# Optimization experiments

Measured on AMD Instinct MI355X. Metric: run time of the kernel, lower is better.

## Reference

```python
import jax, jax.numpy as jnp
import numpy as np

HEADS = 1
EPS = 1e-12  # torch F.normalize eps


def dwt_haar(x):
    # Haar analysis, J=1, zero mode (even H,W -> no padding needed).
    b, c, H, W = x.shape
    xr = x.reshape(b, c, H // 2, 2, W // 2, 2)
    a = xr[:, :, :, 0, :, 0]
    bb = xr[:, :, :, 0, :, 1]
    cc = xr[:, :, :, 1, :, 0]
    d = xr[:, :, :, 1, :, 1]
    ll = (a + bb + cc + d) * 0.5
    h1 = (a - bb + cc - d) * 0.5  # high in width
    h2 = (a + bb - cc - d) * 0.5  # high in height
    h3 = (a - bb - cc + d) * 0.5  # diagonal
    return ll, h1, h2, h3


def idwt_haar(ll, h1, h2, h3):
    a = (ll + h1 + h2 + h3) * 0.5
    bb = (ll - h1 + h2 - h3) * 0.5
    cc = (ll + h1 - h2 - h3) * 0.5
    d = (ll - h1 - h2 + h3) * 0.5
    row0 = jnp.stack([a, bb], axis=-1)   # (b,c,h2,w2,2)
    row1 = jnp.stack([cc, d], axis=-1)
    y = jnp.stack([row0, row1], axis=3)  # (b,c,h2,2,w2,2)
    b_, c_, h2_, _, w2_, _ = y.shape
    return y.reshape(b_, c_, h2_ * 2, w2_ * 2)


def conv1x1(x, w, bias):
    # x: (b,c,h,w); w: (o,c); bias: (o,)
    return jnp.einsum('oc,bchw->bohw', w, x) + bias[None, :, None, None]


def mdta(x, qw, qb, kw, kb, vw, vb, pw, pb, temp):
    b, c, h, w = x.shape
    q = conv1x1(x, qw, qb).reshape(b, HEADS, c // HEADS, h * w)
    k = conv1x1(x, kw, kb).reshape(b, HEADS, c // HEADS, h * w)
    v = conv1x1(x, vw, vb).reshape(b, HEADS, c // HEADS, h * w)
    q = q / jnp.maximum(jnp.linalg.norm(q, axis=-1, keepdims=True), EPS)
    k = k / jnp.maximum(jnp.linalg.norm(k, axis=-1, keepdims=True), EPS)
    attn = jnp.einsum('bhcn,bhdn->bhcd', q, k) * temp[None]
    attn = jax.nn.softmax(attn, axis=-1)
    out = jnp.einsum('bhcd,bhdn->bhcn', attn, v).reshape(b, c, h, w)
    return conv1x1(out, pw, pb)


def setup_inputs() -> dict:
    key = jax.random.key(0)
    ks = jax.random.split(key, 20)
    B, C, H, W = 16, 64, 256, 256
    C3 = 3 * C
    s1 = 1.0 / np.sqrt(C)
    s3 = 1.0 / np.sqrt(C3)
    d = {'img': jax.random.normal(ks[0], (B, C, H, W), jnp.float32)}
    names = ['qw', 'qb', 'kw', 'kb', 'vw', 'vb', 'pw', 'pb']
    for i, n in enumerate(names):
        if n.endswith('w'):
            d['ll_' + n] = jax.random.normal(ks[1 + i], (C, C), jnp.float32) * s1
            d['h_' + n] = jax.random.normal(ks[10 + i], (C3, C3), jnp.float32) * s3
        else:
            d['ll_' + n] = jax.random.normal(ks[1 + i], (C,), jnp.float32) * s1
            d['h_' + n] = jax.random.normal(ks[10 + i], (C3,), jnp.float32) * s3
    d['ll_temp'] = jnp.ones((HEADS, 1, 1), jnp.float32)
    d['h_temp'] = jnp.ones((HEADS, 1, 1), jnp.float32)
    return d


def reference(img, ll_qw, ll_qb, ll_kw, ll_kb, ll_vw, ll_vb, ll_pw, ll_pb, ll_temp,
              h_qw, h_qb, h_kw, h_kb, h_vw, h_vb, h_pw, h_pb, h_temp):
    b, c, H, W = img.shape
    ll, h1, h2, h3 = dwt_haar(img)
    # rearrange 'b c fp h w -> b (c fp) h w' with fp=3 (bands interleaved per channel)
    hh = jnp.stack([h1, h2, h3], axis=2).reshape(b, c * 3, H // 2, W // 2)
    ll = mdta(ll, ll_qw, ll_qb, ll_kw, ll_kb, ll_vw, ll_vb, ll_pw, ll_pb, ll_temp)
    hh = mdta(hh, h_qw, h_qb, h_kw, h_kb, h_vw, h_vb, h_pw, h_pb, h_temp)
    hh = hh.reshape(b, c, 3, H // 2, W // 2)
    return idwt_haar(ll, hh[:, :, 0], hh[:, :, 1], hh[:, :, 2])
```

## Files before the change

kernel.cpp:

```cpp
#include <hip/hip_runtime.h>

typedef __bf16 bf16;
typedef bf16 bf16x8 __attribute__((ext_vector_type(8)));
typedef bf16 bf16x4 __attribute__((ext_vector_type(4)));
typedef float f32x4 __attribute__((ext_vector_type(4)));

#define NB 16
#define CLL 64
#define CHH 192
#define NPIX 16384
#define SL (CLL * CLL)
#define SH (CHH * CHH)

__global__ __launch_bounds__(256) void k_dwt(const float* __restrict__ img, bf16* __restrict__ xll,
                      bf16* __restrict__ xhh, float* __restrict__ sll, float* __restrict__ shh) {
    int bc = blockIdx.y;
    int b = bc >> 6, c = bc & 63;
    int t = threadIdx.x;
    int r = blockIdx.x * 16 + (t >> 4);
    int q = t & 15;
    const float* p0 = img + ((size_t)bc << 16) + (size_t)(2 * r) * 256 + 16 * q;
    const float* p1 = p0 + 256;
    float4 e0[4], e1[4];
    #pragma unroll
    for (int l = 0; l < 4; l++) { e0[l] = ((const float4*)p0)[l]; e1[l] = ((const float4*)p1)[l]; }
    const float* f0 = (const float*)e0;
    const float* f1 = (const float*)e1;
    bf16x8 vll, v1, v2, v3;
    float s0 = 0.f, s1 = 0.f, s2 = 0.f, s3 = 0.f;
    #pragma unroll
    for (int p = 0; p < 8; p++) {
        float a = f0[2 * p], bb = f0[2 * p + 1], cc = f1[2 * p], d = f1[2 * p + 1];
        float wll = (a + bb + cc + d) * 0.5f;
        float w1  = (a - bb + cc - d) * 0.5f;
        float w2  = (a + bb - cc - d) * 0.5f;
        float w3  = (a - bb - cc + d) * 0.5f;
        vll[p] = (bf16)wll; v1[p] = (bf16)w1; v2[p] = (bf16)w2; v3[p] = (bf16)w3;
        s0 += wll; s1 += w1; s2 += w2; s3 += w3;
    }
    size_t n = (size_t)r * 128 + 8 * q;
    *(bf16x8*)(xll + ((size_t)b * CLL + c) * NPIX + n) = vll;
    size_t hb = ((size_t)b * CHH + 3 * c) * NPIX + n;
    *(bf16x8*)(xhh + hb) = v1;
    *(bf16x8*)(xhh + hb + NPIX) = v2;
    *(bf16x8*)(xhh + hb + 2 * NPIX) = v3;
    for (int o = 32; o; o >>= 1) {
        s0 += __shfl_down(s0, o); s1 += __shfl_down(s1, o);
        s2 += __shfl_down(s2, o); s3 += __shfl_down(s3, o);
    }
    if ((t & 63) == 0) {
        atomicAdd(&sll[b * CLL + c], s0);
        atomicAdd(&shh[b * CHH + 3 * c + 0], s1);
        atomicAdd(&shh[b * CHH + 3 * c + 1], s2);
        atomicAdd(&shh[b * CHH + 3 * c + 2], s3);
    }
}

__global__ __launch_bounds__(256) void k_gramv(const bf16* __restrict__ xll,
        const bf16* __restrict__ xhh, float* __restrict__ Gll, float* __restrict__ Ghh,
        const float* __restrict__ llvw, const float* __restrict__ hvw,
        float* __restrict__ vwTll, float* __restrict__ vwThh) {
    __shared__ bf16 sA[64 * 64];
    __shared__ bf16 sB[64 * 64];
    int blk = blockIdx.x, t = threadIdx.x;
    if (blk >= 1024) {
        int base = (blk - 1024) * 256 + t;
        for (int idx = base; idx < SL + SH; idx += 32 * 256) {
            if (idx < SL) {
                int r = idx / CLL, k = idx % CLL;
                vwTll[idx] = llvw[(size_t)k * CLL + r];
            } else {
                int i2 = idx - SL;
                int r = i2 / CHH, k = i2 % CHH;
                vwThh[i2] = hvw[(size_t)k * CHH + r];
            }
        }
        return;
    }
    int C, ti, tj, sk, b2, KC;
    const bf16* X; float* G;
    if (blk < 768) {
        C = CHH; sk = blk % 8; int tl = (blk / 8) % 6; b2 = blk / 48; KC = 2048;
        ti = (tl < 3) ? 0 : ((tl < 5) ? 1 : 2);
        tj = (tl < 3) ? tl : ((tl < 5) ? tl - 2 : 2);
        X = xhh + (size_t)b2 * CHH * NPIX; G = Ghh + (size_t)b2 * SH;
    } else {
        int j = blk - 768;
        C = CLL; sk = j % 16; b2 = j / 16; KC = 1024; ti = 0; tj = 0;
        X = xll + (size_t)b2 * CLL * NPIX; G = Gll + (size_t)b2 * SL;
    }
    int lane = t & 63, wv = t >> 6;
    int g = lane >> 4, l15 = lane & 15;
    int rowi = t >> 3, chunk = t & 7;
    int k0 = sk * KC;
    const bf16* gA0 = X + (size_t)(ti * 64 + rowi) * NPIX + k0 + chunk * 8;
    const bf16* gA1 = gA0 + (size_t)32 * NPIX;
    const bf16* gB0 = X + (size_t)(tj * 64 + rowi) * NPIX + k0 + chunk * 8;
    const bf16* gB1 = gB0 + (size_t)32 * NPIX;
    int swc = (chunk ^ (rowi & 7)) * 8;
    bf16* lA0 = sA + rowi * 64 + swc;
    bf16* lA1 = sA + (rowi + 32) * 64 + swc;
    bf16* lB0 = sB + rowi * 64 + swc;
    bf16* lB1 = sB + (rowi + 32) * 64 + swc;
    int arow = (wv >> 1) * 32;
    int bcol = (wv & 1) * 32;
    int sw = l15 & 7;
    int roA0 = (arow + l15) * 64, roA1 = roA0 + 16 * 64;
    int roB0 = (bcol + l15) * 64, roB1 = roB0 + 16 * 64;
    f32x4 acc[2][2] = {};
    bf16x8 rA0 = *(const bf16x8*)gA0;
    bf16x8 rA1 = *(const bf16x8*)gA1;
    bf16x8 rB0 = *(const bf16x8*)gB0;
    bf16x8 rB1 = *(const bf16x8*)gB1;
    for (int kc = 0; kc < KC; kc += 64) {
        *(bf16x8*)lA0 = rA0; *(bf16x8*)lA1 = rA1;
        *(bf16x8*)lB0 = rB0; *(bf16x8*)lB1 = rB1;
        __syncthreads();
        if (kc + 64 < KC) {
            rA0 = *(const bf16x8*)(gA0 + kc + 64);
            rA1 = *(const bf16x8*)(gA1 + kc + 64);
            rB0 = *(const bf16x8*)(gB0 + kc + 64);
            rB1 = *(const bf16x8*)(gB1 + kc + 64);
        }
        #pragma unroll
        for (int ks = 0; ks < 2; ks++) {
            int ck = ((ks * 4 + g) ^ sw) * 8;
            bf16x8 a0 = *(const bf16x8*)(sA + roA0 + ck);
            bf16x8 a1 = *(const bf16x8*)(sA + roA1 + ck);
            bf16x8 b0 = *(const bf16x8*)(sB + roB0 + ck);
            bf16x8 b1 = *(const bf16x8*)(sB + roB1 + ck);
            acc[0][0] = __builtin_amdgcn_mfma_f32_16x16x32_bf16(a0, b0, acc[0][0], 0, 0, 0);
            acc[0][1] = __builtin_amdgcn_mfma_f32_16x16x32_bf16(a0, b1, acc[0][1], 0, 0, 0);
            acc[1][0] = __builtin_amdgcn_mfma_f32_16x16x32_bf16(a1, b0, acc[1][0], 0, 0, 0);
            acc[1][1] = __builtin_amdgcn_mfma_f32_16x16x32_bf16(a1, b1, acc[1][1], 0, 0, 0);
        }
        __syncthreads();
    }
    int r0q = ti * 64 + arow;
    int c0q = tj * 64 + bcol;
    #pragma unroll
    for (int rr = 0; rr < 2; rr++)
        #pragma unroll
        for (int c2 = 0; c2 < 2; c2++)
            #pragma unroll
            for (int rg = 0; rg < 4; rg++) {
                int row = r0q + rr * 16 + g * 4 + rg;
                int col = c0q + c2 * 16 + l15;
                atomicAdd(&G[(size_t)row * C + col], acc[rr][c2][rg]);
            }
}

__global__ void k_prep2(float* __restrict__ Gll, float* __restrict__ Ghh) {
    int total = NB * (SL + SH);
    for (int idx = blockIdx.x * 256 + threadIdx.x; idx < total; idx += gridDim.x * 256) {
        int b = idx / (SL + SH), r = idx % (SL + SH);
        if (r < SL) {
            float* Gb = Gll + (size_t)b * SL;
            int i = r / CLL, j = r % CLL;
            if (j < i) Gb[r] = Gb[(size_t)j * CLL + i];
        } else {
            int r2 = r - SL;
            float* Gb = Ghh + (size_t)b * SH;
            int i = r2 / CHH, j = r2 % CHH;
            if (j < i) Gb[r2] = Gb[(size_t)j * CHH + i];
        }
    }
}

template <typename OUT>
__global__ __launch_bounds__(256) void k_ntu(
        const float* __restrict__ Xll0, const float* __restrict__ Xll1, long XllbS,
        const float* __restrict__ Yll, long YllbS,
        OUT* __restrict__ Oll, long OllzS, long OllbS,
        const float* __restrict__ Xhh0, const float* __restrict__ Xhh1, long XhhbS,
        const float* __restrict__ Yhh, long YhhbS,
        OUT* __restrict__ Ohh, long OhhzS, long OhhbS) {
    int x = blockIdx.x, b = blockIdx.y, z = blockIdx.z;
    int C, rt, ct;
    const float *X, *Y;
    OUT* O;
    if (x == 0) {
        C = CLL; rt = 0; ct = 0;
        X = (z ? Xll1 : Xll0) + (size_t)b * XllbS;
        Y = Yll + (size_t)b * YllbS;
        O = Oll + (size_t)z * OllzS + (size_t)b * OllbS;
    } else {
        C = CHH; int tl = x - 1; rt = tl / 3; ct = tl % 3;
        X = (z ? Xhh1 : Xhh0) + (size_t)b * XhhbS;
        Y = Yhh + (size_t)b * YhhbS;
        O = Ohh + (size_t)z * OhhzS + (size_t)b * OhhbS;
    }
    int t = threadIdx.x, ti = t >> 4, tj = t & 15;
    const float* xr = X + (size_t)(rt * 64 + ti * 4) * C;
    const float* yr = Y + (size_t)(ct * 64 + tj * 4) * C;
    float acc[4][4] = {};
    for (int k = 0; k < C; k += 4) {
        float4 xa[4], yb[4];
        #pragma unroll
        for (int a = 0; a < 4; a++) xa[a] = *(const float4*)(xr + (size_t)a * C + k);
        #pragma unroll
        for (int q = 0; q < 4; q++) yb[q] = *(const float4*)(yr + (size_t)q * C + k);
        #pragma unroll
        for (int a = 0; a < 4; a++)
            #pragma unroll
            for (int q = 0; q < 4; q++)
                acc[a][q] += xa[a].x * yb[q].x + xa[a].y * yb[q].y
                           + xa[a].z * yb[q].z + xa[a].w * yb[q].w;
    }
    #pragma unroll
    for (int a = 0; a < 4; a++) {
        int row = rt * 64 + ti * 4 + a, col = ct * 64 + tj * 4;
        if constexpr (sizeof(OUT) == 4) {
            *(float4*)((float*)O + (size_t)row * C + col) =
                make_float4(acc[a][0], acc[a][1], acc[a][2], acc[a][3]);
        } else {
            bf16x4 v;
            v[0] = (bf16)acc[a][0]; v[1] = (bf16)acc[a][1];
            v[2] = (bf16)acc[a][2]; v[3] = (bf16)acc[a][3];
            *(bf16x4*)((bf16*)O + (size_t)row * C + col) = v;
        }
    }
}

__global__ __launch_bounds__(256) void k_nrm(const float* __restrict__ PRll,
        const float* __restrict__ PRhh,
        const float* __restrict__ llqw, const float* __restrict__ llkw,
        const float* __restrict__ hqw,  const float* __restrict__ hkw,
        const float* __restrict__ llqb, const float* __restrict__ llkb,
        const float* __restrict__ hqb,  const float* __restrict__ hkb,
        const float* __restrict__ sll,  const float* __restrict__ shh,
        float* __restrict__ nrmll, float* __restrict__ nrmhh,
        float* __restrict__ wsll,  float* __restrict__ wshh) {
    int z = blockIdx.z, b = blockIdx.y;
    int wv = threadIdx.x >> 6, lane = threadIdx.x & 63;
    int gr = blockIdx.x * 4 + wv;
    int C, i; const float *P, *w, *wb, *s; float *nrm, *ws;
    if (gr < CLL) {
        C = CLL; i = gr;
        P = PRll + ((size_t)z * NB + b) * SL;
        w = z ? llkw : llqw; wb = z ? llkb : llqb;
        s = sll + (size_t)b * CLL;
        nrm = nrmll + ((size_t)z * NB + b) * CLL;
        ws  = wsll  + ((size_t)z * NB + b) * CLL;
    } else {
        C = CHH; i = gr - CLL;
        P = PRhh + ((size_t)z * NB + b) * SH;
        w = z ? hkw : hqw; wb = z ? hkb : hqb;
        s = shh + (size_t)b * CHH;
        nrm = nrmhh + ((size_t)z * NB + b) * CHH;
        ws  = wshh  + ((size_t)z * NB + b) * CHH;
    }
    const float* Pi = P + (size_t)i * C;
    const float* wi = w + (size_t)i * C;
    float np = 0.f, sd = 0.f;
    for (int j = lane; j < C; j += 64) {
        float wj = wi[j];
        np += Pi[j] * wj;
        sd += wj * s[j];
    }
    for (int o = 32; o; o >>= 1) { np += __shfl_down(np, o); sd += __shfl_down(sd, o); }
    if (lane == 0) {
        float wbi = wb[i];
        float q2 = np + 2.f * wbi * sd + (float)NPIX * wbi * wbi;
        nrm[i] = fmaxf(sqrtf(fmaxf(q2, 0.f)), 1e-12f);
        ws[i] = sd;
    }
}

__global__ __launch_bounds__(256) void k_soft2(
        const float* __restrict__ Lll, const float* __restrict__ Lhh,
        const float* __restrict__ llkb, const float* __restrict__ llqb,
        const float* __restrict__ hkb,  const float* __restrict__ hqb,
        const float* __restrict__ nrmll, const float* __restrict__ nrmhh,
        const float* __restrict__ wsll,  const float* __restrict__ wshh,
        const float* __restrict__ llvb,  const float* __restrict__ hvb,
        const float* __restrict__ lltp,  const float* __restrict__ htp,
        float* __restrict__ All, float* __restrict__ Ahh,
        float* __restrict__ avll, float* __restrict__ avhh) {
    int b = blockIdx.y;
    int wv = threadIdx.x >> 6, lane = threadIdx.x & 63;
    int gr = blockIdx.x * 4 + wv;
    int C, i; const float *Lb, *kb, *qb, *qn, *kn, *qs, *ks, *vb, *tp;
    float *A, *av;
    if (gr < CLL) {
        C = CLL; i = gr;
        Lb = Lll + (size_t)b * SL; kb = llkb; qb = llqb;
        qn = nrmll + (size_t)b * CLL;  kn = nrmll + ((size_t)NB + b) * CLL;
        qs = wsll + (size_t)b * CLL;   ks = wsll + ((size_t)NB + b) * CLL;
        vb = llvb; tp = lltp;
        A = All + (size_t)b * SL; av = avll + (size_t)b * CLL;
    } else {
        C = CHH; i = gr - CLL;
        Lb = Lhh + (size_t)b * SH; kb = hkb; qb = hqb;
        qn = nrmhh + (size_t)b * CHH;  kn = nrmhh + ((size_t)NB + b) * CHH;
        qs = wshh + (size_t)b * CHH;   ks = wshh + ((size_t)NB + b) * CHH;
        vb = hvb; tp = htp;
        A = Ahh + (size_t)b * SH; av = avhh + (size_t)b * CHH;
    }
    const float* Li = Lb + (size_t)i * C;
    float qni = qn[i], qsi = qs[i], qbi = qb[i], tmp = tp[0];
    float Lv[3];
    #pragma unroll
    for (int s2 = 0; s2 < 3; s2++) {
        int j = lane + s2 * 64;
        if (j < C) {
            float l = Li[j] + qsi * kb[j] + qbi * ks[j] + (float)NPIX * qbi * kb[j];
            Lv[s2] = l / (qni * kn[j]) * tmp;
        } else Lv[s2] = -1e30f;
    }
    float mx = fmaxf(fmaxf(Lv[0], Lv[1]), Lv[2]);
    for (int o = 32; o; o >>= 1) mx = fmaxf(mx, __shfl_xor(mx, o));
    float e[3], sum = 0.f;
    #pragma unroll
    for (int s2 = 0; s2 < 3; s2++) {
        e[s2] = (lane + s2 * 64 < C) ? expf(Lv[s2] - mx) : 0.f;
        sum += e[s2];
    }
    for (int o = 32; o; o >>= 1) sum += __shfl_xor(sum, o);
    float inv = 1.f / sum;
    float avp = 0.f;
    #pragma unroll
    for (int s2 = 0; s2 < 3; s2++) {
        int j = lane + s2 * 64;
        if (j < C) {
            float a = e[s2] * inv;
            A[(size_t)i * C + j] = a;
            avp += a * vb[j];
        }
    }
    for (int o = 32; o; o >>= 1) avp += __shfl_down(avp, o);
    if (lane == 0) av[i] = avp;
}

__global__ __launch_bounds__(256) void k_mv(const float* __restrict__ llpw,
        const float* __restrict__ llpb, const float* __restrict__ hpw,
        const float* __restrict__ hpb, const float* __restrict__ avll,
        const float* __restrict__ avhh, float* __restrict__ mvll, float* __restrict__ mvhh) {
    int b = blockIdx.y;
    int wv = threadIdx.x >> 6, lane = threadIdx.x & 63;
    int gr = blockIdx.x * 4 + wv;
    int C, i; const float *pw, *pb_, *av_; float* mv_;
    if (gr < CLL) {
        C = CLL; i = gr;
        pw = llpw; pb_ = llpb; av_ = avll + (size_t)b * CLL; mv_ = mvll + (size_t)b * CLL;
    } else {
        C = CHH; i = gr - CLL;
        pw = hpw; pb_ = hpb; av_ = avhh + (size_t)b * CHH; mv_ = mvhh + (size_t)b * CHH;
    }
    const float* pwi = pw + (size_t)i * C;
    float m = 0.f;
    for (int k = lane; k < C; k += 64) m += pwi[k] * av_[k];
    for (int o = 32; o; o >>= 1) m += __shfl_down(m, o);
    if (lane == 0) mv_[i] = m + pb_[i];
}

__global__ __launch_bounds__(256) void k_final(const bf16* __restrict__ xll, const bf16* __restrict__ xhh,
                        const bf16* __restrict__ Mll, const bf16* __restrict__ Mhh,
                        const float* __restrict__ mvll, const float* __restrict__ mvhh,
                        float* __restrict__ out) {
    __shared__ alignas(16) float smemf[256 * 65];
    bf16* sxl = (bf16*)smemf;
    bf16* sxh = (bf16*)smemf + 64 * 64;
    float* Y = smemf;
    int b = blockIdx.y, tile = blockIdx.x;
    int irow = tile >> 1, j0 = (tile & 1) << 6;
    int n0 = irow * 128 + j0;
    int t = threadIdx.x;
    const bf16* Xl = xll + (size_t)b * CLL * NPIX;
    const bf16* Xh = xhh + (size_t)b * CHH * NPIX;
    for (int task = t; task < 512; task += 256) {
        int d = task >> 3, q = task & 7;
        bf16x8 v = *(const bf16x8*)(Xl + (size_t)d * NPIX + n0 + q * 8);
        int cs = (((d >> 3) ^ q) << 3) | (d & 7);
        #pragma unroll
        for (int p = 0; p < 8; p++) sxl[(q * 8 + p) * 64 + cs] = v[p];
    }
    for (int task = t; task < 1536; task += 256) {
        int d = task >> 3, q = task & 7;
        bf16x8 v = *(const bf16x8*)(Xh + (size_t)d * NPIX + n0 + q * 8);
        int c = d >> 3;
        int cs = ((((c & ~7) | ((c & 7) ^ q))) << 3) | (d & 7);
        #pragma unroll
        for (int p = 0; p < 8; p++) sxh[(q * 8 + p) * 192 + cs] = v[p];
    }
    __syncthreads();
    int wv = t >> 6, lane = t & 63, g = lane >> 4, l15 = lane & 15;
    f32x4 accL[4] = {};
    {
        const bf16* M = Mll + (size_t)b * SL + (size_t)(wv * 16 + l15) * CLL;
        #pragma unroll
        for (int ks = 0; ks < 2; ks++) {
            bf16x8 af = *(const bf16x8*)(M + ks * 32 + g * 8);
            int cc = ks * 4 + g;
            #pragma unroll
            for (int c2 = 0; c2 < 4; c2++) {
                int pxr = c2 * 16 + l15;
                int csw = cc ^ ((pxr >> 3) & 7);
                bf16x8 bfrag = *(const bf16x8*)(sxl + pxr * 64 + csw * 8);
                accL[c2] = __builtin_amdgcn_mfma_f32_16x16x32_bf16(af, bfrag, accL[c2], 0, 0, 0);
            }
        }
    }
    f32x4 accH[3][4] = {};
    {
        const bf16* M = Mhh + (size_t)b * SH;
        #pragma unroll 2
        for (int kb = 0; kb < CHH; kb += 32) {
            bf16x8 af[3];
            #pragma unroll
            for (int r = 0; r < 3; r++)
                af[r] = *(const bf16x8*)(M + (size_t)(wv * 48 + r * 16 + l15) * CHH + kb + g * 8);
            #pragma unroll
            for (int c2 = 0; c2 < 4; c2++) {
                int pxr = c2 * 16 + l15;
                int cc = (kb >> 3) + g;
                int csw = (cc & ~7) | ((cc & 7) ^ ((pxr >> 3) & 7));
                bf16x8 bfrag = *(const bf16x8*)(sxh + pxr * 192 + csw * 8);
                #pragma unroll
                for (int r = 0; r < 3; r++)
                    accH[r][c2] = __builtin_amdgcn_mfma_f32_16x16x32_bf16(af[r], bfrag, accH[r][c2], 0, 0, 0);
            }
        }
    }
    __syncthreads();
    #pragma unroll
    for (int c2 = 0; c2 < 4; c2++)
        #pragma unroll
        for (int rg = 0; rg < 4; rg++) {
            int rl = wv * 16 + g * 4 + rg;
            Y[rl * 65 + c2 * 16 + l15] = accL[c2][rg] + mvll[b * CLL + rl];
        }
    #pragma unroll
    for (int r = 0; r < 3; r++)
        #pragma unroll
        for (int c2 = 0; c2 < 4; c2++)
            #pragma unroll
            for (int rg = 0; rg < 4; rg++) {
                int rh = wv * 48 + r * 16 + g * 4 + rg;
                Y[(64 + rh) * 65 + c2 * 16 + l15] = accH[r][c2][rg] + mvhh[b * CHH + rh];
            }
    __syncthreads();
    int p = t & 63, cg = t >> 6;
    float* ob = out + ((size_t)b * CLL) * 65536;
    for (int it = 0; it < 16; it++) {
        int c = it * 4 + cg;
        float ll = Y[c * 65 + p];
        float h1 = Y[(64 + 3 * c + 0) * 65 + p];
        float h2 = Y[(64 + 3 * c + 1) * 65 + p];
        float h3 = Y[(64 + 3 * c + 2) * 65 + p];
        float a  = (ll + h1 + h2 + h3) * 0.5f;
        float bb = (ll - h1 + h2 - h3) * 0.5f;
        float cc = (ll + h1 - h2 - h3) * 0.5f;
        float d  = (ll - h1 - h2 + h3) * 0.5f;
        int jj = j0 + p;
        float2* o0 = (float2*)(ob + ((size_t)c * 256 + 2 * irow) * 256 + 2 * jj);
        float2* o1 = (float2*)(ob + ((size_t)c * 256 + 2 * irow + 1) * 256 + 2 * jj);
        *o0 = make_float2(a, bb);
        *o1 = make_float2(cc, d);
    }
}

extern "C" void kernel_launch(void* const* d_in, const int* in_sizes, int n_in,
                              void* d_out, int out_size, void* d_ws, size_t ws_size,
                              hipStream_t stream) {
    const float* img    = (const float*)d_in[0];
    const float* ll_qw = (const float*)d_in[1];  const float* h_qw = (const float*)d_in[2];
    const float* ll_qb = (const float*)d_in[3];  const float* h_qb = (const float*)d_in[4];
    const float* ll_kw = (const float*)d_in[5];  const float* h_kw = (const float*)d_in[6];
    const float* ll_kb = (const float*)d_in[7];  const float* h_kb = (const float*)d_in[8];
    const float* ll_vw = (const float*)d_in[9];  const float* h_vw = (const float*)d_in[10];
    const float* ll_vb = (const float*)d_in[11]; const float* h_vb = (const float*)d_in[12];
    const float* ll_pw = (const float*)d_in[13]; const float* h_pw = (const float*)d_in[14];
    const float* ll_pb = (const float*)d_in[15]; const float* h_pb = (const float*)d_in[16];
    const float* ll_tp = (const float*)d_in[17]; const float* h_tp = (const float*)d_in[18];
    float* out = (float*)d_out;

    char* ws = (char*)d_ws;
    size_t off = 0;
    auto alloc = [&](size_t sz) { char* p = ws + off; off += (sz + 255) & ~(size_t)255; return p; };
    bf16*  xll  = (bf16*) alloc((size_t)NB * CLL * NPIX * 2);
    bf16*  xhh  = (bf16*) alloc((size_t)NB * CHH * NPIX * 2);
    char*  zb   = ws + off;
    float* sll  = (float*)alloc(NB * CLL * 4);
    float* shh  = (float*)alloc(NB * CHH * 4);
    float* Gll  = (float*)alloc((size_t)NB * SL * 4);
    float* Ghh  = (float*)alloc((size_t)NB * SH * 4);
    size_t zsz  = (size_t)((ws + off) - zb);
    float* PRll = (float*)alloc(2 * (size_t)NB * SL * 4);
    float* PRhh = (float*)alloc(2 * (size_t)NB * SH * 4);
    float* nrmll= (float*)alloc(2 * NB * CLL * 4);
    float* nrmhh= (float*)alloc(2 * NB * CHH * 4);
    float* wsll = (float*)alloc(2 * NB * CLL * 4);
    float* wshh = (float*)alloc(2 * NB * CHH * 4);
    float* Lll  = (float*)alloc((size_t)NB * SL * 4);
    float* Lhh  = (float*)alloc((size_t)NB * SH * 4);
    float* All  = (float*)alloc((size_t)NB * SL * 4);
    float* Ahh  = (float*)alloc((size_t)NB * SH * 4);
    float* avll = (float*)alloc(NB * CLL * 4);   float* avhh = (float*)alloc(NB * CHH * 4);
    float* WTll = (float*)alloc((size_t)NB * SL * 4);
    float* WThh = (float*)alloc((size_t)NB * SH * 4);
    float* vwTll= (float*)alloc(SL * 4);
    float* vwThh= (float*)alloc(SH * 4);
    bf16*  Mll  = (bf16*) alloc((size_t)NB * SL * 2);
    bf16*  Mhh  = (bf16*) alloc((size_t)NB * SH * 2);
    float* mvll = (float*)alloc(NB * CLL * 4);   float* mvhh = (float*)alloc(NB * CHH * 4);

    hipMemsetAsync(zb, 0, zsz, stream);

    k_dwt<<<dim3(8, NB * 64), 256, 0, stream>>>(img, xll, xhh, sll, shh);

    k_gramv<<<1056, 256, 0, stream>>>(xll, xhh, Gll, Ghh, ll_vw, h_vw, vwTll, vwThh);

    k_prep2<<<1024, 256, 0, stream>>>(Gll, Ghh);

    k_ntu<float><<<dim3(10, NB, 2), 256, 0, stream>>>(
        ll_qw, ll_kw, 0, Gll, (long)SL, PRll, (long)NB * SL, (long)SL,
        h_qw,  h_kw,  0, Ghh, (long)SH, PRhh, (long)NB * SH, (long)SH);

    k_nrm<<<dim3(64, NB, 2), 256, 0, stream>>>(PRll, PRhh,
        ll_qw, ll_kw, h_qw, h_kw, ll_qb, ll_kb, h_qb, h_kb, sll, shh,
        nrmll, nrmhh, wsll, wshh);

    k_ntu<float><<<dim3(10, NB, 1), 256, 0, stream>>>(
        PRll, PRll, (long)SL, ll_kw, 0, Lll, 0, (long)SL,
        PRhh, PRhh, (long)SH, h_kw,  0, Lhh, 0, (long)SH);

    k_soft2<<<dim3(64, NB), 256, 0, stream>>>(Lll, Lhh, ll_kb, ll_qb, h_kb, h_qb,
        nrmll, nrmhh, wsll, wshh, ll_vb, h_vb, ll_tp, h_tp, All, Ahh, avll, avhh);

    k_mv<<<dim3(64, NB), 256, 0, stream>>>(ll_pw, ll_pb, h_pw, h_pb, avll, avhh, mvll, mvhh);

    k_ntu<float><<<dim3(10, NB, 1), 256, 0, stream>>>(
        vwTll, vwTll, 0, All, (long)SL, WTll, 0, (long)SL,
        vwThh, vwThh, 0, Ahh, (long)SH, WThh, 0, (long)SH);

    k_ntu<bf16><<<dim3(10, NB, 1), 256, 0, stream>>>(
        ll_pw, ll_pw, 0, WTll, (long)SL, Mll, 0, (long)SL,
        h_pw,  h_pw,  0, WThh, (long)SH, Mhh, 0, (long)SH);

    k_final<<<dim3(256, NB), 256, 0, stream>>>(xll, xhh, Mll, Mhh, mvll, mvhh, out);
}
```

Before: 424.6 us.

## Fuse small reduction kernels with GEMM kernels and drop Gram symmetrize pass

```diff
diff --git a/kernel.cpp b/kernel.cpp
--- a/kernel.cpp
+++ b/kernel.cpp
@@ -138,6 +138,7 @@
     }
     int r0q = ti * 64 + arow;
     int c0q = tj * 64 + bcol;
+    bool offd = (ti != tj);
     #pragma unroll
     for (int rr = 0; rr < 2; rr++)
         #pragma unroll
@@ -146,25 +147,10 @@
             for (int rg = 0; rg < 4; rg++) {
                 int row = r0q + rr * 16 + g * 4 + rg;
                 int col = c0q + c2 * 16 + l15;
-                atomicAdd(&G[(size_t)row * C + col], acc[rr][c2][rg]);
+                float v = acc[rr][c2][rg];
+                atomicAdd(&G[(size_t)row * C + col], v);
+                if (offd) atomicAdd(&G[(size_t)col * C + row], v);
             }
-}
-
-__global__ void k_prep2(float* __restrict__ Gll, float* __restrict__ Ghh) {
-    int total = NB * (SL + SH);
-    for (int idx = blockIdx.x * 256 + threadIdx.x; idx < total; idx += gridDim.x * 256) {
-        int b = idx / (SL + SH), r = idx % (SL + SH);
-        if (r < SL) {
-            float* Gb = Gll + (size_t)b * SL;
-            int i = r / CLL, j = r % CLL;
-            if (j < i) Gb[r] = Gb[(size_t)j * CLL + i];
-        } else {
-            int r2 = r - SL;
-            float* Gb = Ghh + (size_t)b * SH;
-            int i = r2 / CHH, j = r2 % CHH;
-            if (j < i) Gb[r2] = Gb[(size_t)j * CHH + i];
-        }
-    }
 }
 
 template <typename OUT>
@@ -222,48 +208,84 @@
     }
 }
 
-__global__ __launch_bounds__(256) void k_nrm(const float* __restrict__ PRll,
-        const float* __restrict__ PRhh,
+__global__ __launch_bounds__(256) void k_lnrm(
+        const float* __restrict__ PRll, const float* __restrict__ PRhh,
         const float* __restrict__ llqw, const float* __restrict__ llkw,
         const float* __restrict__ hqw,  const float* __restrict__ hkw,
         const float* __restrict__ llqb, const float* __restrict__ llkb,
         const float* __restrict__ hqb,  const float* __restrict__ hkb,
         const float* __restrict__ sll,  const float* __restrict__ shh,
         float* __restrict__ nrmll, float* __restrict__ nrmhh,
-        float* __restrict__ wsll,  float* __restrict__ wshh) {
-    int z = blockIdx.z, b = blockIdx.y;
-    int wv = threadIdx.x >> 6, lane = threadIdx.x & 63;
-    int gr = blockIdx.x * 4 + wv;
-    int C, i; const float *P, *w, *wb, *s; float *nrm, *ws;
-    if (gr < CLL) {
-        C = CLL; i = gr;
-        P = PRll + ((size_t)z * NB + b) * SL;
-        w = z ? llkw : llqw; wb = z ? llkb : llqb;
-        s = sll + (size_t)b * CLL;
-        nrm = nrmll + ((size_t)z * NB + b) * CLL;
-        ws  = wsll  + ((size_t)z * NB + b) * CLL;
+        float* __restrict__ wsll,  float* __restrict__ wshh,
+        float* __restrict__ Lll, float* __restrict__ Lhh) {
+    int blk = blockIdx.x, t = threadIdx.x;
+    int wvv = t >> 6, lane = t & 63;
+    for (int wt = blk * 4 + wvv; wt < 8192; wt += 640) {
+        int z = wt >> 12, b2 = (wt >> 8) & 15, gr = wt & 255;
+        int C, i; const float *P, *w, *wb, *s; float *nrm, *ws;
+        if (gr < CLL) {
+            C = CLL; i = gr;
+            P = PRll + ((size_t)z * NB + b2) * SL;
+            w = z ? llkw : llqw; wb = z ? llkb : llqb;
+            s = sll + (size_t)b2 * CLL;
+            nrm = nrmll + ((size_t)z * NB + b2) * CLL;
+            ws  = wsll  + ((size_t)z * NB + b2) * CLL;
+        } else {
+            C = CHH; i = gr - CLL;
+            P = PRhh + ((size_t)z * NB + b2) * SH;
+            w = z ? hkw : hqw; wb = z ? hkb : hqb;
+            s = shh + (size_t)b2 * CHH;
+            nrm = nrmhh + ((size_t)z * NB + b2) * CHH;
+            ws  = wshh  + ((size_t)z * NB + b2) * CHH;
+        }
+        const float* Pi = P + (size_t)i * C;
+        const float* wi = w + (size_t)i * C;
+        float np = 0.f, sd = 0.f;
+        for (int j = lane; j < C; j += 64) {
+            float wj = wi[j];
+            np += Pi[j] * wj;
+            sd += wj * s[j];
+        }
+        for (int o = 32; o; o >>= 1) { np += __shfl_down(np, o); sd += __shfl_down(sd, o); }
+        if (lane == 0) {
+            float wbi = wb[i];
+            float q2 = np + 2.f * wbi * sd + (float)NPIX * wbi * wbi;
+            nrm[i] = fmaxf(sqrtf(fmaxf(q2, 0.f)), 1e-12f);
+            ws[i] = sd;
+        }
+    }
+    int x = blk % 10, b = blk / 10;
+    int C, rt, ct;
+    const float *X, *Y; float* O;
+    if (x == 0) {
+        C = CLL; rt = 0; ct = 0;
+        X = PRll + (size_t)b * SL; Y = llkw; O = Lll + (size_t)b * SL;
     } else {
-        C = CHH; i = gr - CLL;
-        P = PRhh + ((size_t)z * NB + b) * SH;
-        w = z ? hkw : hqw; wb = z ? hkb : hqb;
-        s = shh + (size_t)b * CHH;
-        nrm = nrmhh + ((size_t)z * NB + b) * CHH;
-        ws  = wshh  + ((size_t)z * NB + b) * CHH;
-    }
-    const float* Pi = P + (size_t)i * C;
-    const float* wi = w + (size_t)i * C;
-    float np = 0.f, sd = 0.f;
-    for (int j = lane; j < C; j += 64) {
-        float wj = wi[j];
-        np += Pi[j] * wj;
-        sd += wj * s[j];
-    }
-    for (int o = 32; o; o >>= 1) { np += __shfl_down(np, o); sd += __shfl_down(sd, o); }
-    if (lane == 0) {
-        float wbi = wb[i];
-        float q2 = np + 2.f * wbi * sd + (float)NPIX * wbi * wbi;
-        nrm[i] = fmaxf(sqrtf(fmaxf(q2, 0.f)), 1e-12f);
-        ws[i] = sd;
+        C = CHH; int tl = x - 1; rt = tl / 3; ct = tl % 3;
+        X = PRhh + (size_t)b * SH; Y = hkw; O = Lhh + (size_t)b * SH;
+    }
+    int ti = t >> 4, tj = t & 15;
+    const float* xr = X + (size_t)(rt * 64 + ti * 4) * C;
+    const float* yr = Y + (size_t)(ct * 64 + tj * 4) * C;
+    float acc[4][4] = {};
+    for (int k = 0; k < C; k += 4) {
+        float4 xa[4], yb[4];
+        #pragma unroll
+        for (int a = 0; a < 4; a++) xa[a] = *(const float4*)(xr + (size_t)a * C + k);
+        #pragma unroll
+        for (int q = 0; q < 4; q++) yb[q] = *(const float4*)(yr + (size_t)q * C + k);
+        #pragma unroll
+        for (int a = 0; a < 4; a++)
+            #pragma unroll
+            for (int q = 0; q < 4; q++)
+                acc[a][q] += xa[a].x * yb[q].x + xa[a].y * yb[q].y
+                           + xa[a].z * yb[q].z + xa[a].w * yb[q].w;
+    }
+    #pragma unroll
+    for (int a = 0; a < 4; a++) {
+        int row = rt * 64 + ti * 4 + a, col = ct * 64 + tj * 4;
+        *(float4*)(O + (size_t)row * C + col) =
+            make_float4(acc[a][0], acc[a][1], acc[a][2], acc[a][3]);
     }
 }
 
@@ -332,26 +354,65 @@
     if (lane == 0) av[i] = avp;
 }
 
-__global__ __launch_bounds__(256) void k_mv(const float* __restrict__ llpw,
-        const float* __restrict__ llpb, const float* __restrict__ hpw,
-        const float* __restrict__ hpb, const float* __restrict__ avll,
-        const float* __restrict__ avhh, float* __restrict__ mvll, float* __restrict__ mvhh) {
-    int b = blockIdx.y;
-    int wv = threadIdx.x >> 6, lane = threadIdx.x & 63;
-    int gr = blockIdx.x * 4 + wv;
-    int C, i; const float *pw, *pb_, *av_; float* mv_;
-    if (gr < CLL) {
-        C = CLL; i = gr;
-        pw = llpw; pb_ = llpb; av_ = avll + (size_t)b * CLL; mv_ = mvll + (size_t)b * CLL;
+__global__ __launch_bounds__(256) void k_wtmv(
+        const float* __restrict__ vwTll, const float* __restrict__ vwThh,
+        const float* __restrict__ All, const float* __restrict__ Ahh,
+        const float* __restrict__ llpw, const float* __restrict__ llpb,
+        const float* __restrict__ hpw,  const float* __restrict__ hpb,
+        const float* __restrict__ avll, const float* __restrict__ avhh,
+        float* __restrict__ WTll, float* __restrict__ WThh,
+        float* __restrict__ mvll, float* __restrict__ mvhh) {
+    int blk = blockIdx.x, t = threadIdx.x;
+    int wvv = t >> 6, lane = t & 63;
+    for (int wt = blk * 4 + wvv; wt < 4096; wt += 640) {
+        int b2 = wt >> 8, gr = wt & 255;
+        int C, i; const float *pw, *pb_, *av_; float* mv_;
+        if (gr < CLL) {
+            C = CLL; i = gr;
+            pw = llpw; pb_ = llpb; av_ = avll + (size_t)b2 * CLL; mv_ = mvll + (size_t)b2 * CLL;
+        } else {
+            C = CHH; i = gr - CLL;
+            pw = hpw; pb_ = hpb; av_ = avhh + (size_t)b2 * CHH; mv_ = mvhh + (size_t)b2 * CHH;
+        }
+        const float* pwi = pw + (size_t)i * C;
+        float m = 0.f;
+        for (int k = lane; k < C; k += 64) m += pwi[k] * av_[k];
+        for (int o = 32; o; o >>= 1) m += __shfl_down(m, o);
+        if (lane == 0) mv_[i] = m + pb_[i];
+    }
+    int x = blk % 10, b = blk / 10;
+    int C, rt, ct;
+    const float *X, *Y; float* O;
+    if (x == 0) {
+        C = CLL; rt = 0; ct = 0;
+        X = vwTll; Y = All + (size_t)b * SL; O = WTll + (size_t)b * SL;
     } else {
-        C = CHH; i = gr - CLL;
-        pw = hpw; pb_ = hpb; av_ = avhh + (size_t)b * CHH; mv_ = mvhh + (size_t)b * CHH;
-    }
-    const float* pwi = pw + (size_t)i * C;
-    float m = 0.f;
-    for (int k = lane; k < C; k += 64) m += pwi[k] * av_[k];
-    for (int o = 32; o; o >>= 1) m += __shfl_down(m, o);
-    if (lane == 0) mv_[i] = m + pb_[i];
+        C = CHH; int tl = x - 1; rt = tl / 3; ct = tl % 3;
+        X = vwThh; Y = Ahh + (size_t)b * SH; O = WThh + (size_t)b * SH;
+    }
+    int ti = t >> 4, tj = t & 15;
+    const float* xr = X + (size_t)(rt * 64 + ti * 4) * C;
+    const float* yr = Y + (size_t)(ct * 64 + tj * 4) * C;
+    float acc[4][4] = {};
+    for (int k = 0; k < C; k += 4) {
+        float4 xa[4], yb[4];
+        #pragma unroll
+        for (int a = 0; a < 4; a++) xa[a] = *(const float4*)(xr + (size_t)a * C + k);
+        #pragma unroll
+        for (int q = 0; q < 4; q++) yb[q] = *(const float4*)(yr + (size_t)q * C + k);
+        #pragma unroll
+        for (int a = 0; a < 4; a++)
+            #pragma unroll
+            for (int q = 0; q < 4; q++)
+                acc[a][q] += xa[a].x * yb[q].x + xa[a].y * yb[q].y
+                           + xa[a].z * yb[q].z + xa[a].w * yb[q].w;
+    }
+    #pragma unroll
+    for (int a = 0; a < 4; a++) {
+        int row = rt * 64 + ti * 4 + a, col = ct * 64 + tj * 4;
+        *(float4*)(O + (size_t)row * C + col) =
+            make_float4(acc[a][0], acc[a][1], acc[a][2], acc[a][3]);
+    }
 }
 
 __global__ __launch_bounds__(256) void k_final(const bf16* __restrict__ xll, const bf16* __restrict__ xhh,
@@ -511,28 +572,19 @@
 
     k_gramv<<<1056, 256, 0, stream>>>(xll, xhh, Gll, Ghh, ll_vw, h_vw, vwTll, vwThh);
 
-    k_prep2<<<1024, 256, 0, stream>>>(Gll, Ghh);
-
     k_ntu<float><<<dim3(10, NB, 2), 256, 0, stream>>>(
         ll_qw, ll_kw, 0, Gll, (long)SL, PRll, (long)NB * SL, (long)SL,
         h_qw,  h_kw,  0, Ghh, (long)SH, PRhh, (long)NB * SH, (long)SH);
 
-    k_nrm<<<dim3(64, NB, 2), 256, 0, stream>>>(PRll, PRhh,
+    k_lnrm<<<160, 256, 0, stream>>>(PRll, PRhh,
         ll_qw, ll_kw, h_qw, h_kw, ll_qb, ll_kb, h_qb, h_kb, sll, shh,
-        nrmll, nrmhh, wsll, wshh);
-
-    k_ntu<float><<<dim3(10, NB, 1), 256, 0, stream>>>(
-        PRll, PRll, (long)SL, ll_kw, 0, Lll, 0, (long)SL,
-        PRhh, PRhh, (long)SH, h_kw,  0, Lhh, 0, (long)SH);
+        nrmll, nrmhh, wsll, wshh, Lll, Lhh);
 
     k_soft2<<<dim3(64, NB), 256, 0, stream>>>(Lll, Lhh, ll_kb, ll_qb, h_kb, h_qb,
         nrmll, nrmhh, wsll, wshh, ll_vb, h_vb, ll_tp, h_tp, All, Ahh, avll, avhh);
 
-    k_mv<<<dim3(64, NB), 256, 0, stream>>>(ll_pw, ll_pb, h_pw, h_pb, avll, avhh, mvll, mvhh);
-
-    k_ntu<float><<<dim3(10, NB, 1), 256, 0, stream>>>(
-        vwTll, vwTll, 0, All, (long)SL, WTll, 0, (long)SL,
-        vwThh, vwThh, 0, Ahh, (long)SH, WThh, 0, (long)SH);
+    k_wtmv<<<160, 256, 0, stream>>>(vwTll, vwThh, All, Ahh,
+        ll_pw, ll_pb, h_pw, h_pb, avll, avhh, WTll, WThh, mvll, mvhh);
 
     k_ntu<bf16><<<dim3(10, NB, 1), 256, 0, stream>>>(
         ll_pw, ll_pw, 0, WTll, (long)SL, Mll, 0, (long)SL,
```

After: 460.1 us. 1.08x slower.
